# Performance work log

Hardware: AMD Instinct MI355X
Metric: run time of the kernel (lower is better)

Reference implementation:

```python
import jax, jax.numpy as jnp
import numpy as np

B, S, D, H, C, E, V = 8, 2048, 1024, 512, 256, 64, 64


def setup_inputs() -> dict:
    key = jax.random.key(0)
    ks = jax.random.split(key, 40)
    ri = lambda i, hi: jax.random.randint(ks[i], (B, S), 0, hi).astype(jnp.int32)
    p = lambda i, shape: (jax.random.normal(ks[i], shape, jnp.float32) * 0.02)
    inp = {
        'h_x': jax.random.normal(ks[0], (B, S, D), jnp.float32),
        'h_y': jax.random.normal(ks[1], (B, S, D), jnp.float32),
        'x_mask': jnp.ones((B, S), jnp.int32),
        'y_mask': jnp.ones((B, S), jnp.int32),
        'src_token_dense_mask': ri(2, 2), 'src_token_sparse_mask': ri(3, 2),
        'src_token_inarc_type': ri(4, V), 'src_token_arc_head': ri(5, S),
        'src_token_depth': ri(6, 16), 'src_word_inarc_type': ri(7, V),
        'src_word_inarc_type_mask': ri(8, 2),
        'tgt_token_dense_mask': ri(9, 2), 'tgt_token_sparse_mask': ri(10, 2),
        'tgt_token_inarc_type': ri(11, V), 'tgt_token_arc_head': ri(12, S),
        'tgt_token_depth': ri(13, 16), 'tgt_word_inarc_type': ri(14, V),
        'tgt_word_inarc_type_mask': ri(15, 2),
        # src MLP [D->H->C], tgt MLP [D->H->C]
        'W1s': p(16, (D, H)), 'b1s': jnp.zeros((H,), jnp.float32),
        'W2s': p(17, (H, C)), 'b2s': jnp.zeros((C,), jnp.float32),
        'W1t': p(18, (D, H)), 'b1t': jnp.zeros((H,), jnp.float32),
        'W2t': p(19, (H, C)), 'b2t': jnp.zeros((C,), jnp.float32),
        # inarc edge embedding + GeneralConv params
        'emb': p(20, (V, E)),
        'W_msg': p(21, (C, C)), 'b_msg': jnp.zeros((C,), jnp.float32),
        'W_edge': p(22, (E, C)),
        'att': p(23, (C,)),
        'W_self': p(24, (C, C)), 'b_self': jnp.zeros((C,), jnp.float32),
        # axis_feature MLP [C->C]
        'Wf': p(25, (C, C)), 'bf': jnp.zeros((C,), jnp.float32),
    }
    return inp


def _mlp(h, W1, b1, W2, b2):
    return jax.nn.leaky_relu(h @ W1 + b1) @ W2 + b2


def _graph_side(h, dense_m, sparse_m, arc_head, word_type, word_mask,
                W1, b1, W2, b2, emb, W_msg, b_msg, W_edge, att, W_self, b_self, Wf, bf):
    Bn, Sn, _ = h.shape
    x = _mlp(h, W1, b1, W2, b2)                      # [B,S,C]
    N = Bn * Sn
    Cn = x.shape[-1]
    xg = x.reshape(N, Cn)                            # debatch -> nodes
    off = (jnp.arange(Bn, dtype=jnp.int32) * Sn)[:, None]
    src = (arc_head + off).reshape(N)                # global head index per token
    dst = jnp.arange(N, dtype=jnp.int32)             # one in-edge per token
    valid = (sparse_m * dense_m).reshape(N).astype(x.dtype)
    ef = emb[(word_type * word_mask).reshape(N)]     # [N,E] edge embeddings
    # GeneralConv: directed message with edge features + additive attention
    m = xg[src] @ W_msg + b_msg + ef @ W_edge        # [N,C] messages
    hd = xg @ W_msg + b_msg                          # dst-side term for attention
    logit = jax.nn.leaky_relu(((m + hd) * att).sum(-1))
    logit = jnp.where(valid > 0, logit, -1e9)
    emax = jax.ops.segment_max(logit, dst, num_segments=N)
    ex = jnp.exp(logit - emax[dst]) * valid
    den = jax.ops.segment_sum(ex, dst, num_segments=N)
    alpha = ex / (den[dst] + 1e-16)                  # softmax per destination node
    agg = jax.ops.segment_sum(m * alpha[:, None], dst, num_segments=N)
    out = xg @ W_self + b_self + agg                 # skip_linear
    out = out / jnp.maximum(jnp.linalg.norm(out, axis=-1, keepdims=True), 1e-12)
    r = out.reshape(Bn, Sn, Cn).mean(axis=1, keepdims=True)  # FeatureRepr mean
    return r @ Wf + bf                               # [B,1,C]


def reference(h_x, x_mask, src_token_dense_mask, src_token_sparse_mask,
              src_token_inarc_type, src_token_arc_head, src_token_depth,
              src_word_inarc_type, src_word_inarc_type_mask,
              h_y, y_mask, tgt_token_dense_mask, tgt_token_sparse_mask,
              tgt_token_inarc_type, tgt_token_arc_head, tgt_token_depth,
              tgt_word_inarc_type, tgt_word_inarc_type_mask,
              W1s, b1s, W2s, b2s, W1t, b1t, W2t, b2t,
              emb, W_msg, b_msg, W_edge, att, W_self, b_self, Wf, bf):
    src_repr = _graph_side(h_x, src_token_dense_mask, src_token_sparse_mask,
                           src_token_arc_head, src_word_inarc_type, src_word_inarc_type_mask,
                           W1s, b1s, W2s, b2s, emb, W_msg, b_msg, W_edge, att,
                           W_self, b_self, Wf, bf)
    tgt_repr = _graph_side(h_y, tgt_token_dense_mask, tgt_token_sparse_mask,
                           tgt_token_arc_head, tgt_word_inarc_type, tgt_word_inarc_type_mask,
                           W1t, b1t, W2t, b2t, emb, W_msg, b_msg, W_edge, att,
                           W_self, b_self, Wf, bf)
    return (src_repr, tgt_repr)
```

## Files before the change

### kernel.cpp

```cpp
#include <hip/hip_runtime.h>
#include <stdint.h>

#define SEQ   2048
#define NNODE 16384

typedef short  short8  __attribute__((ext_vector_type(8)));
typedef float  float4v __attribute__((ext_vector_type(4)));
typedef unsigned short u16;
typedef unsigned short u16x8 __attribute__((ext_vector_type(8)));
typedef short  short4v __attribute__((ext_vector_type(4)));

__device__ __forceinline__ float b2f(u16 u) {
    union { unsigned int i; float f; } x; x.i = ((unsigned int)u) << 16; return x.f;
}
__device__ __forceinline__ u16 f2b(float f) {
    union { float f; unsigned int i; } x; x.f = f;
    unsigned int u = x.i;
    unsigned int r = (u + 0x7fffu + ((u >> 16) & 1u)) >> 16;
    return (u16)r;
}

__device__ __forceinline__ void gld16(const void* g, void* l) {
    __builtin_amdgcn_global_load_lds(
        (const __attribute__((address_space(1))) void*)g,
        (__attribute__((address_space(3))) void*)l, 16, 0, 0);
}

struct GemmP {
    const void*  A[2];
    const u16*   B[2];
    const float* bias[2];
    u16*         out[2];
};

#define LDW 136

template <int ACT, int AF32>
__global__ __launch_bounds__(256) void gemm_k(GemmP p, int M, int N, int K) {
    __shared__ __align__(16) u16 smem[128 * LDW];
    u16* As = smem;
    u16* Bs = smem + 8192;

    const int z = blockIdx.z;
    const u16*   __restrict__ B    = p.B[z];
    const float* __restrict__ bias = p.bias[z];

    const int mt  = blockIdx.x * 128;
    const int nt  = blockIdx.y * 128;
    const int tid = threadIdx.x;
    const int l   = tid & 63;
    const int w   = tid >> 6;
    const int wm  = (w >> 1) * 64;
    const int wn  = (w & 1) * 64;
    const int lr  = l & 15;
    const int lk  = l >> 4;

    float4v acc[4][4] = {};

    for (int k0 = 0; k0 < K; k0 += 64) {
#pragma unroll
        for (int it = 0; it < 4; ++it) {
            int f  = it * 256 + tid;
            int rm = f >> 3, cc = f & 7;
            int gc = cc ^ (rm & 7);
            if (AF32) {
                const float* __restrict__ A32 = (const float*)p.A[z];
                const float* src = A32 + (size_t)(mt + rm) * K + (k0 + cc * 8);
                float4v a = *(const float4v*)src;
                float4v b = *(const float4v*)(src + 4);
                u16x8 r;
                r[0] = f2b(a[0]); r[1] = f2b(a[1]); r[2] = f2b(a[2]); r[3] = f2b(a[3]);
                r[4] = f2b(b[0]); r[5] = f2b(b[1]); r[6] = f2b(b[2]); r[7] = f2b(b[3]);
                *(u16x8*)(As + ((size_t)rm * 8 + (cc ^ (rm & 7))) * 8) = r;
            } else {
                const u16* __restrict__ A16 = (const u16*)p.A[z];
                gld16(A16 + (size_t)(mt + rm) * K + (k0 + gc * 8),
                      As + (size_t)f * 8);
            }
            gld16(B + (size_t)(nt + rm) * K + (k0 + gc * 8), Bs + (size_t)f * 8);
        }
        __syncthreads();
#pragma unroll
        for (int ks = 0; ks < 2; ++ks) {
            short8 af[4], bfr[4];
            const int kc = ks * 4 + lk;
#pragma unroll
            for (int i = 0; i < 4; ++i) {
                int ra = wm + i * 16 + lr;
                af[i]  = *(const short8*)(As + ((size_t)ra * 8 + (kc ^ (ra & 7))) * 8);
                int rb = wn + i * 16 + lr;
                bfr[i] = *(const short8*)(Bs + ((size_t)rb * 8 + (kc ^ (rb & 7))) * 8);
            }
#pragma unroll
            for (int i = 0; i < 4; ++i)
#pragma unroll
                for (int j = 0; j < 4; ++j)
                    acc[i][j] = __builtin_amdgcn_mfma_f32_16x16x32_bf16(
                        af[i], bfr[j], acc[i][j], 0, 0, 0);
        }
        __syncthreads();
    }

    const int r0 = lk * 4;
#pragma unroll
    for (int j = 0; j < 4; ++j) {
        const int lc = wn + j * 16 + lr;
        const float bv = bias[nt + lc];
#pragma unroll
        for (int i = 0; i < 4; ++i) {
            const int lrow = wm + i * 16 + r0;
#pragma unroll
            for (int r = 0; r < 4; ++r) {
                float v = acc[i][j][r] + bv;
                if (ACT) v = v > 0.f ? v : 0.01f * v;
                smem[(size_t)(lrow + r) * LDW + lc] = f2b(v);
            }
        }
    }
    __syncthreads();
#pragma unroll
    for (int pass = 0; pass < 8; ++pass) {
        int id   = pass * 256 + tid;
        int row  = id >> 4, colc = id & 15;
        u16x8 vv = *(const u16x8*)(smem + (size_t)row * LDW + colc * 8);
        *(u16x8*)(p.out[z] + (size_t)(mt + row) * N + nt + colc * 8) = vv;
    }
}

struct TP { const float* src[6]; u16* dst[6]; int K[6]; int N[6]; };

__global__ __launch_bounds__(256) void transpose_k(TP t) {
    __shared__ float tile[64][65];
    const int m = blockIdx.y;
    const int K = t.K[m], N = t.N[m];
    const int tn = N >> 6;
    const int ntiles = (K >> 6) * tn;
    const int bid = blockIdx.x;
    if (bid >= ntiles) return;
    const int k0 = (bid / tn) * 64, n0 = (bid % tn) * 64;
    const int tid = threadIdx.x;
#pragma unroll
    for (int pass = 0; pass < 4; ++pass) {
        int kk = pass * 16 + (tid >> 4);
        int nn = (tid & 15) * 4;
        float4v v = *(const float4v*)(t.src[m] + (size_t)(k0 + kk) * N + n0 + nn);
        tile[kk][nn + 0] = v[0]; tile[kk][nn + 1] = v[1];
        tile[kk][nn + 2] = v[2]; tile[kk][nn + 3] = v[3];
    }
    __syncthreads();
    const int n = tid >> 2, kc = (tid & 3) * 16;
    u16x8 a, b;
#pragma unroll
    for (int j = 0; j < 8; ++j) {
        a[j] = f2b(tile[kc + j][n]);
        b[j] = f2b(tile[kc + 8 + j][n]);
    }
    u16* d = t.dst[m] + (size_t)(n0 + n) * K + k0 + kc;
    *(u16x8*)d = a;
    *(u16x8*)(d + 8) = b;
}

__global__ void ew_k(const float* emb, const float* W_edge, float* EW) {
    const int t = blockIdx.x, c = threadIdx.x;
    float s = 0.f;
    for (int e = 0; e < 64; ++e)
        s += emb[t * 64 + e] * W_edge[e * 256 + c];
    EW[t * 256 + c] = s;
}

__global__ void bias_cat_k(const float* bmsg, const float* bself, float* bcat) {
    const int tid = threadIdx.x;
    bcat[tid]       = bmsg[tid];
    bcat[256 + tid] = bself[tid];
}

struct EpiP {
    const u16* xcat[2];
    const int* den[2]; const int* spa[2]; const int* arc[2];
    const int* wty[2]; const int* wma[2];
    const float* EW; float* racc;
};

__global__ __launch_bounds__(256) void epi_k(EpiP p) {
    __shared__ float part[4][256];
    const int bx    = blockIdx.x;
    const int side  = bx >> 9;
    const int local = bx & 511;
    const int base  = local * 32;
    const int b     = base >> 11;
    const int tid   = threadIdx.x;
    const int w = tid >> 6, l = tid & 63;

    const u16* __restrict__ xcat = p.xcat[side];

    float4v acc = {};
    for (int j = 0; j < 8; ++j) {
        const int i     = base + w * 8 + j;
        const int valid = p.den[side][i] * p.spa[side][i];
        const int srcn  = p.arc[side][i] + (i >> 11) * SEQ;
        const int t     = p.wty[side][i] * p.wma[side][i];
        short4v xs = *(const short4v*)(xcat + (size_t)i * 512 + 256 + l * 4);
        short4v xm = *(const short4v*)(xcat + (size_t)srcn * 512 + l * 4);
        float4v ew = *(const float4v*)(p.EW + (size_t)t * 256 + l * 4);
        const float vm = valid ? 1.f : 0.f;
        float4v v;
        v[0] = b2f((u16)xs[0]) + vm * (b2f((u16)xm[0]) + ew[0]);
        v[1] = b2f((u16)xs[1]) + vm * (b2f((u16)xm[1]) + ew[1]);
        v[2] = b2f((u16)xs[2]) + vm * (b2f((u16)xm[2]) + ew[2]);
        v[3] = b2f((u16)xs[3]) + vm * (b2f((u16)xm[3]) + ew[3]);
        float ss = v[0]*v[0] + v[1]*v[1] + v[2]*v[2] + v[3]*v[3];
        for (int m = 32; m >= 1; m >>= 1) ss += __shfl_xor(ss, m, 64);
        const float rn = 1.f / fmaxf(sqrtf(ss), 1e-12f);
        acc[0] += v[0] * rn; acc[1] += v[1] * rn;
        acc[2] += v[2] * rn; acc[3] += v[3] * rn;
    }
    part[w][l * 4 + 0] = acc[0];
    part[w][l * 4 + 1] = acc[1];
    part[w][l * 4 + 2] = acc[2];
    part[w][l * 4 + 3] = acc[3];
    __syncthreads();
    const float s = part[0][tid] + part[1][tid] + part[2][tid] + part[3][tid];
    atomicAdd(p.racc + ((size_t)side * 8 + b) * 256 + tid, s);
}

__global__ void fin_k(const float* racc, const float* Wf, const float* bfv,
                      float* out) {
    __shared__ float r[256];
    const int bid = blockIdx.x;
    const int tid = threadIdx.x;
    r[tid] = racc[bid * 256 + tid] * (1.f / 2048.f);
    __syncthreads();
    float s = bfv[tid];
    for (int k = 0; k < 256; ++k)
        s += r[k] * Wf[k * 256 + tid];
    out[bid * 256 + tid] = s;
}

extern "C" void kernel_launch(void* const* d_in, const int* in_sizes, int n_in,
                              void* d_out, int out_size, void* d_ws, size_t ws_size,
                              hipStream_t stream) {
    const float* h[2]   = {(const float*)d_in[0],  (const float*)d_in[1]};
    const int* den[2]   = {(const int*)d_in[4],  (const int*)d_in[11]};
    const int* spa[2]   = {(const int*)d_in[5],  (const int*)d_in[12]};
    const int* arc[2]   = {(const int*)d_in[7],  (const int*)d_in[14]};
    const int* wty[2]   = {(const int*)d_in[9],  (const int*)d_in[16]};
    const int* wma[2]   = {(const int*)d_in[10], (const int*)d_in[17]};
    const float* W1[2]  = {(const float*)d_in[18], (const float*)d_in[22]};
    const float* b1[2]  = {(const float*)d_in[19], (const float*)d_in[23]};
    const float* W2[2]  = {(const float*)d_in[20], (const float*)d_in[24]};
    const float* b2[2]  = {(const float*)d_in[21], (const float*)d_in[25]};
    const float* emb    = (const float*)d_in[26];
    const float* Wmsg   = (const float*)d_in[27];
    const float* bmsg   = (const float*)d_in[28];
    const float* Wedge  = (const float*)d_in[29];
    const float* Wself  = (const float*)d_in[31];
    const float* bself  = (const float*)d_in[32];
    const float* Wf     = (const float*)d_in[33];
    const float* bf_    = (const float*)d_in[34];

    char* ws = (char*)d_ws;
    size_t off = 0;
    auto alloc = [&](size_t bytes) -> void* {
        void* pp = ws + off; off += (bytes + 255) & ~(size_t)255; return pp;
    };
    u16*   x1    = (u16*)  alloc(2ull * NNODE * 512 * 2);
    u16*   xx    = (u16*)  alloc(2ull * NNODE * 256 * 2);
    u16*   xcat  = (u16*)  alloc(2ull * NNODE * 512 * 2);
    u16*   W1T   = (u16*)  alloc(2ull * 512 * 1024 * 2);
    u16*   W2T   = (u16*)  alloc(2ull * 256 * 512 * 2);
    u16*   WcatT = (u16*)  alloc(512 * 256 * 2);
    float* EW    = (float*)alloc(64 * 256 * 4);
    float* bcat  = (float*)alloc(512 * 4);
    float* racc  = (float*)alloc(2 * 8 * 256 * 4);

    TP tp;
    tp.src[0] = W1[0]; tp.dst[0] = W1T;              tp.K[0] = 1024; tp.N[0] = 512;
    tp.src[1] = W1[1]; tp.dst[1] = W1T + 512 * 1024; tp.K[1] = 1024; tp.N[1] = 512;
    tp.src[2] = W2[0]; tp.dst[2] = W2T;              tp.K[2] = 512;  tp.N[2] = 256;
    tp.src[3] = W2[1]; tp.dst[3] = W2T + 256 * 512;  tp.K[3] = 512;  tp.N[3] = 256;
    tp.src[4] = Wmsg;  tp.dst[4] = WcatT;            tp.K[4] = 256;  tp.N[4] = 256;
    tp.src[5] = Wself; tp.dst[5] = WcatT + 256*256;  tp.K[5] = 256;  tp.N[5] = 256;
    hipLaunchKernelGGL(transpose_k, dim3(128, 6), dim3(256), 0, stream, tp);
    hipLaunchKernelGGL(ew_k, dim3(64), dim3(256), 0, stream, emb, Wedge, EW);
    hipLaunchKernelGGL(bias_cat_k, dim3(1), dim3(256), 0, stream, bmsg, bself, bcat);
    hipMemsetAsync(racc, 0, 2 * 8 * 256 * 4, stream);

    GemmP g1 = {};
    g1.A[0] = h[0];  g1.A[1] = h[1];
    g1.B[0] = W1T;   g1.B[1] = W1T + 512 * 1024;
    g1.bias[0] = b1[0]; g1.bias[1] = b1[1];
    g1.out[0] = x1;  g1.out[1] = x1 + (size_t)NNODE * 512;
    hipLaunchKernelGGL((gemm_k<1, 1>), dim3(128, 4, 2), dim3(256), 0, stream,
                       g1, NNODE, 512, 1024);

    GemmP g2 = {};
    g2.A[0] = x1;  g2.A[1] = x1 + (size_t)NNODE * 512;
    g2.B[0] = W2T; g2.B[1] = W2T + 256 * 512;
    g2.bias[0] = b2[0]; g2.bias[1] = b2[1];
    g2.out[0] = xx; g2.out[1] = xx + (size_t)NNODE * 256;
    hipLaunchKernelGGL((gemm_k<0, 0>), dim3(128, 2, 2), dim3(256), 0, stream,
                       g2, NNODE, 256, 512);

    GemmP g3 = {};
    g3.A[0] = xx;    g3.A[1] = xx + (size_t)NNODE * 256;
    g3.B[0] = WcatT; g3.B[1] = WcatT;
    g3.bias[0] = bcat; g3.bias[1] = bcat;
    g3.out[0] = xcat;  g3.out[1] = xcat + (size_t)NNODE * 512;
    hipLaunchKernelGGL((gemm_k<0, 0>), dim3(128, 4, 2), dim3(256), 0, stream,
                       g3, NNODE, 512, 256);

    EpiP ep;
    ep.xcat[0] = xcat; ep.xcat[1] = xcat + (size_t)NNODE * 512;
    for (int s = 0; s < 2; ++s) {
        ep.den[s] = den[s]; ep.spa[s] = spa[s]; ep.arc[s] = arc[s];
        ep.wty[s] = wty[s]; ep.wma[s] = wma[s];
    }
    ep.EW = EW; ep.racc = racc;
    hipLaunchKernelGGL(epi_k, dim3(1024), dim3(256), 0, stream, ep);

    hipLaunchKernelGGL(fin_k, dim3(16), dim3(256), 0, stream,
                       racc, Wf, bf_, (float*)d_out);
}
```

Measured before the change: 319.8 us.

## Double-buffer GEMM LDS tiles to overlap global loads with MFMA compute

The GEMM main loop now uses two LDS buffers of 64 KB total. The next K-slice is issued into the alternate buffer, either by global_load_lds for bf16 A and B or by a register prefetch for fp32 A, before the MFMA work on the current slice. This removes one barrier per iteration and aims to hide global load latency behind compute. It doubles shared memory and adds prefetch registers, and launch_bounds(256,2) is added, which may limit occupancy or cause spills.

```diff
diff --git a/kernel.cpp b/kernel.cpp
--- a/kernel.cpp
+++ b/kernel.cpp
@@ -36,14 +36,14 @@
 #define LDW 136
 
 template <int ACT, int AF32>
-__global__ __launch_bounds__(256) void gemm_k(GemmP p, int M, int N, int K) {
-    __shared__ __align__(16) u16 smem[128 * LDW];
-    u16* As = smem;
-    u16* Bs = smem + 8192;
+__global__ __launch_bounds__(256, 2) void gemm_k(GemmP p, int M, int N, int K) {
+    __shared__ __align__(16) u16 smem[32768];
 
     const int z = blockIdx.z;
     const u16*   __restrict__ B    = p.B[z];
     const float* __restrict__ bias = p.bias[z];
+    const u16*   __restrict__ A16  = (const u16*)p.A[z];
+    const float* __restrict__ A32  = (const float*)p.A[z];
 
     const int mt  = blockIdx.x * 128;
     const int nt  = blockIdx.y * 128;
@@ -56,30 +56,61 @@
     const int lk  = l >> 4;
 
     float4v acc[4][4] = {};
-
-    for (int k0 = 0; k0 < K; k0 += 64) {
+    float4v pa[8];
+
+    auto stageB = [&](int k0, u16* Bs) {
 #pragma unroll
         for (int it = 0; it < 4; ++it) {
-            int f  = it * 256 + tid;
-            int rm = f >> 3, cc = f & 7;
-            int gc = cc ^ (rm & 7);
-            if (AF32) {
-                const float* __restrict__ A32 = (const float*)p.A[z];
-                const float* src = A32 + (size_t)(mt + rm) * K + (k0 + cc * 8);
-                float4v a = *(const float4v*)src;
-                float4v b = *(const float4v*)(src + 4);
-                u16x8 r;
-                r[0] = f2b(a[0]); r[1] = f2b(a[1]); r[2] = f2b(a[2]); r[3] = f2b(a[3]);
-                r[4] = f2b(b[0]); r[5] = f2b(b[1]); r[6] = f2b(b[2]); r[7] = f2b(b[3]);
-                *(u16x8*)(As + ((size_t)rm * 8 + (cc ^ (rm & 7))) * 8) = r;
-            } else {
-                const u16* __restrict__ A16 = (const u16*)p.A[z];
-                gld16(A16 + (size_t)(mt + rm) * K + (k0 + gc * 8),
-                      As + (size_t)f * 8);
-            }
+            int f = it * 256 + tid, rm = f >> 3, cc = f & 7, gc = cc ^ (rm & 7);
             gld16(B + (size_t)(nt + rm) * K + (k0 + gc * 8), Bs + (size_t)f * 8);
         }
-        __syncthreads();
+    };
+    auto stageA16 = [&](int k0, u16* As) {
+#pragma unroll
+        for (int it = 0; it < 4; ++it) {
+            int f = it * 256 + tid, rm = f >> 3, cc = f & 7, gc = cc ^ (rm & 7);
+            gld16(A16 + (size_t)(mt + rm) * K + (k0 + gc * 8), As + (size_t)f * 8);
+        }
+    };
+    auto prefA32 = [&](int k0) {
+#pragma unroll
+        for (int it = 0; it < 4; ++it) {
+            int f = it * 256 + tid, rm = f >> 3, cc = f & 7;
+            const float* s = A32 + (size_t)(mt + rm) * K + k0 + cc * 8;
+            pa[2 * it]     = *(const float4v*)s;
+            pa[2 * it + 1] = *(const float4v*)(s + 4);
+        }
+    };
+    auto cvtWrite = [&](u16* As) {
+#pragma unroll
+        for (int it = 0; it < 4; ++it) {
+            int f = it * 256 + tid, rm = f >> 3, cc = f & 7;
+            float4v a = pa[2 * it], b = pa[2 * it + 1];
+            u16x8 r;
+            r[0] = f2b(a[0]); r[1] = f2b(a[1]); r[2] = f2b(a[2]); r[3] = f2b(a[3]);
+            r[4] = f2b(b[0]); r[5] = f2b(b[1]); r[6] = f2b(b[2]); r[7] = f2b(b[3]);
+            *(u16x8*)(As + ((size_t)rm * 8 + (cc ^ (rm & 7))) * 8) = r;
+        }
+    };
+
+    const int niter = K >> 6;
+
+    if (AF32) { prefA32(0); cvtWrite(smem); }
+    else      { stageA16(0, smem); }
+    stageB(0, smem + 8192);
+    __syncthreads();
+
+    for (int ki = 0; ki < niter; ++ki) {
+        u16* curb = smem + (ki & 1) * 16384;
+        u16* nxtb = smem + ((ki & 1) ^ 1) * 16384;
+        const bool more = (ki + 1) < niter;
+        if (more) {
+            if (AF32) prefA32((ki + 1) * 64);
+            else      stageA16((ki + 1) * 64, nxtb);
+            stageB((ki + 1) * 64, nxtb + 8192);
+        }
+        const u16* As = curb;
+        const u16* Bs = curb + 8192;
 #pragma unroll
         for (int ks = 0; ks < 2; ++ks) {
             short8 af[4], bfr[4];
@@ -98,6 +129,7 @@
                     acc[i][j] = __builtin_amdgcn_mfma_f32_16x16x32_bf16(
                         af[i], bfr[j], acc[i][j], 0, 0, 0);
         }
+        if (AF32 && more) cvtWrite(nxtb);
         __syncthreads();
     }
 
@@ -120,8 +152,8 @@
     __syncthreads();
 #pragma unroll
     for (int pass = 0; pass < 8; ++pass) {
-        int id   = pass * 256 + tid;
-        int row  = id >> 4, colc = id & 15;
+        int id  = pass * 256 + tid;
+        int row = id >> 4, colc = id & 15;
         u16x8 vv = *(const u16x8*)(smem + (size_t)row * LDW + colc * 8);
         *(u16x8*)(p.out[z] + (size_t)(mt + row) * N + nt + colc * 8) = vv;
     }
```

Measured after the change: 314.1 us. About the same (-1.8%).

## Double-buffer B tiles in GEMM, load A directly to registers, fuse prep kernels

Applied to the files above, without the earlier changes.

The GEMM kernel now double-buffers the B tile in LDS, prefetching the next K slice while computing the current one. A fragments, including the fp32-to-bf16 conversion, are loaded straight from global memory into registers instead of being staged through LDS. Launch-bounds occupancy hints are added per template variant. The separate transpose, edge-weight, bias-concat kernels and the memset are merged into one prep kernel to cut launch count, at the cost of uncoalesced per-lane A loads from global memory.

```diff
diff --git a/kernel.cpp b/kernel.cpp
--- a/kernel.cpp
+++ b/kernel.cpp
@@ -36,14 +36,15 @@
 #define LDW 136
 
 template <int ACT, int AF32>
-__global__ __launch_bounds__(256) void gemm_k(GemmP p, int M, int N, int K) {
+__global__ __launch_bounds__(256, AF32 ? 3 : 4)
+void gemm_k(GemmP p, int M, int N, int K) {
     __shared__ __align__(16) u16 smem[128 * LDW];
-    u16* As = smem;
-    u16* Bs = smem + 8192;
 
     const int z = blockIdx.z;
     const u16*   __restrict__ B    = p.B[z];
     const float* __restrict__ bias = p.bias[z];
+    const u16*   __restrict__ A16  = (const u16*)p.A[z];
+    const float* __restrict__ A32  = (const float*)p.A[z];
 
     const int mt  = blockIdx.x * 128;
     const int nt  = blockIdx.y * 128;
@@ -57,46 +58,60 @@
 
     float4v acc[4][4] = {};
 
-    for (int k0 = 0; k0 < K; k0 += 64) {
+    auto stageB = [&](int k0, u16* Bs) {
 #pragma unroll
         for (int it = 0; it < 4; ++it) {
-            int f  = it * 256 + tid;
-            int rm = f >> 3, cc = f & 7;
-            int gc = cc ^ (rm & 7);
-            if (AF32) {
-                const float* __restrict__ A32 = (const float*)p.A[z];
-                const float* src = A32 + (size_t)(mt + rm) * K + (k0 + cc * 8);
-                float4v a = *(const float4v*)src;
-                float4v b = *(const float4v*)(src + 4);
-                u16x8 r;
-                r[0] = f2b(a[0]); r[1] = f2b(a[1]); r[2] = f2b(a[2]); r[3] = f2b(a[3]);
-                r[4] = f2b(b[0]); r[5] = f2b(b[1]); r[6] = f2b(b[2]); r[7] = f2b(b[3]);
-                *(u16x8*)(As + ((size_t)rm * 8 + (cc ^ (rm & 7))) * 8) = r;
-            } else {
-                const u16* __restrict__ A16 = (const u16*)p.A[z];
-                gld16(A16 + (size_t)(mt + rm) * K + (k0 + gc * 8),
-                      As + (size_t)f * 8);
-            }
+            int f = it * 256 + tid, rm = f >> 3, cc = f & 7, gc = cc ^ (rm & 7);
             gld16(B + (size_t)(nt + rm) * K + (k0 + gc * 8), Bs + (size_t)f * 8);
         }
-        __syncthreads();
+    };
+
+    const int niter = K >> 6;
+
+    stageB(0, smem);
+    __syncthreads();
+
+    for (int ki = 0; ki < niter; ++ki) {
+        const int k0 = ki * 64;
+        u16* cur = smem + (ki & 1) * 8192;
+        u16* nxt = smem + ((ki & 1) ^ 1) * 8192;
+        if (ki + 1 < niter) stageB(k0 + 64, nxt);
+
+        short8 af[2][4];
+#pragma unroll
+        for (int ks = 0; ks < 2; ++ks)
+#pragma unroll
+            for (int i = 0; i < 4; ++i) {
+                const size_t row = (size_t)(mt + wm + i * 16 + lr);
+                const int    kk  = k0 + ks * 32 + lk * 8;
+                if (AF32) {
+                    const float* s = A32 + row * K + kk;
+                    float4v a = *(const float4v*)s;
+                    float4v b = *(const float4v*)(s + 4);
+                    u16x8 r;
+                    r[0] = f2b(a[0]); r[1] = f2b(a[1]); r[2] = f2b(a[2]); r[3] = f2b(a[3]);
+                    r[4] = f2b(b[0]); r[5] = f2b(b[1]); r[6] = f2b(b[2]); r[7] = f2b(b[3]);
+                    af[ks][i] = (short8)r;
+                } else {
+                    af[ks][i] = *(const short8*)(A16 + row * K + kk);
+                }
+            }
+
 #pragma unroll
         for (int ks = 0; ks < 2; ++ks) {
-            short8 af[4], bfr[4];
+            short8 bfr[4];
             const int kc = ks * 4 + lk;
 #pragma unroll
-            for (int i = 0; i < 4; ++i) {
-                int ra = wm + i * 16 + lr;
-                af[i]  = *(const short8*)(As + ((size_t)ra * 8 + (kc ^ (ra & 7))) * 8);
-                int rb = wn + i * 16 + lr;
-                bfr[i] = *(const short8*)(Bs + ((size_t)rb * 8 + (kc ^ (rb & 7))) * 8);
+            for (int j = 0; j < 4; ++j) {
+                int rb = wn + j * 16 + lr;
+                bfr[j] = *(const short8*)(cur + ((size_t)rb * 8 + (kc ^ (rb & 7))) * 8);
             }
 #pragma unroll
             for (int i = 0; i < 4; ++i)
 #pragma unroll
                 for (int j = 0; j < 4; ++j)
                     acc[i][j] = __builtin_amdgcn_mfma_f32_16x16x32_bf16(
-                        af[i], bfr[j], acc[i][j], 0, 0, 0);
+                        af[ks][i], bfr[j], acc[i][j], 0, 0, 0);
         }
         __syncthreads();
     }
@@ -120,8 +135,8 @@
     __syncthreads();
 #pragma unroll
     for (int pass = 0; pass < 8; ++pass) {
-        int id   = pass * 256 + tid;
-        int row  = id >> 4, colc = id & 15;
+        int id  = pass * 256 + tid;
+        int row = id >> 4, colc = id & 15;
         u16x8 vv = *(const u16x8*)(smem + (size_t)row * LDW + colc * 8);
         *(u16x8*)(p.out[z] + (size_t)(mt + row) * N + nt + colc * 8) = vv;
     }
@@ -129,16 +144,40 @@
 
 struct TP { const float* src[6]; u16* dst[6]; int K[6]; int N[6]; };
 
-__global__ __launch_bounds__(256) void transpose_k(TP t) {
+__global__ __launch_bounds__(256) void prep_k(TP t, const float* emb,
+                                              const float* Wedge, float* EW,
+                                              const float* bmsg, const float* bself,
+                                              float* bcat, float* racc) {
     __shared__ float tile[64][65];
     const int m = blockIdx.y;
     const int K = t.K[m], N = t.N[m];
     const int tn = N >> 6;
     const int ntiles = (K >> 6) * tn;
     const int bid = blockIdx.x;
-    if (bid >= ntiles) return;
+    const int tid = threadIdx.x;
+    if (bid >= ntiles) {
+        if (m == 5) {
+            int extra = bid - ntiles;
+            if (extra < 16) {
+                int tt = extra * 4 + (tid >> 6);
+                int c  = (tid & 63) * 4;
+                float4v s = {};
+                for (int e = 0; e < 64; ++e) {
+                    float ev = emb[tt * 64 + e];
+                    float4v wr = *(const float4v*)(Wedge + e * 256 + c);
+                    s[0] += ev * wr[0]; s[1] += ev * wr[1];
+                    s[2] += ev * wr[2]; s[3] += ev * wr[3];
+                }
+                *(float4v*)(EW + tt * 256 + c) = s;
+            } else if (extra == 16) {
+                bcat[tid]       = bmsg[tid];
+                bcat[256 + tid] = bself[tid];
+                for (int i = tid; i < 4096; i += 256) racc[i] = 0.f;
+            }
+        }
+        return;
+    }
     const int k0 = (bid / tn) * 64, n0 = (bid % tn) * 64;
-    const int tid = threadIdx.x;
 #pragma unroll
     for (int pass = 0; pass < 4; ++pass) {
         int kk = pass * 16 + (tid >> 4);
@@ -158,20 +197,6 @@
     u16* d = t.dst[m] + (size_t)(n0 + n) * K + k0 + kc;
     *(u16x8*)d = a;
     *(u16x8*)(d + 8) = b;
-}
-
-__global__ void ew_k(const float* emb, const float* W_edge, float* EW) {
-    const int t = blockIdx.x, c = threadIdx.x;
-    float s = 0.f;
-    for (int e = 0; e < 64; ++e)
-        s += emb[t * 64 + e] * W_edge[e * 256 + c];
-    EW[t * 256 + c] = s;
-}
-
-__global__ void bias_cat_k(const float* bmsg, const float* bself, float* bcat) {
-    const int tid = threadIdx.x;
-    bcat[tid]       = bmsg[tid];
-    bcat[256 + tid] = bself[tid];
 }
 
 struct EpiP {
@@ -280,10 +305,8 @@
     tp.src[3] = W2[1]; tp.dst[3] = W2T + 256 * 512;  tp.K[3] = 512;  tp.N[3] = 256;
     tp.src[4] = Wmsg;  tp.dst[4] = WcatT;            tp.K[4] = 256;  tp.N[4] = 256;
     tp.src[5] = Wself; tp.dst[5] = WcatT + 256*256;  tp.K[5] = 256;  tp.N[5] = 256;
-    hipLaunchKernelGGL(transpose_k, dim3(128, 6), dim3(256), 0, stream, tp);
-    hipLaunchKernelGGL(ew_k, dim3(64), dim3(256), 0, stream, emb, Wedge, EW);
-    hipLaunchKernelGGL(bias_cat_k, dim3(1), dim3(256), 0, stream, bmsg, bself, bcat);
-    hipMemsetAsync(racc, 0, 2 * 8 * 256 * 4, stream);
+    hipLaunchKernelGGL(prep_k, dim3(128, 6), dim3(256), 0, stream, tp,
+                       emb, Wedge, EW, bmsg, bself, bcat, racc);
 
     GemmP g1 = {};
     g1.A[0] = h[0];  g1.A[1] = h[1];
```

Result: slower. 405.8 us (+26.9%).
